# Performance work log

Hardware: AMD Instinct MI355X
Metric: run time of the kernel (lower is better)

The kernel has to match this reference:

```python
import jax, jax.numpy as jnp
import numpy as np

# Module config (matches init_kwargs shape_data=[8,32,32], pow=1, spde_type='adv_diff')
N_T, N_Y, N_X = 8, 32, 32
N = N_Y * N_X            # nb_nodes
DX = DY = DT = 1.0


def build_A(kappa, m1, m2, h11, h12, h22):
    """Dense [N,N] advection-diffusion operator A = kappa^2 I + m.grad - div(H grad),
    central differences on the n_y x n_x grid, zero-Dirichlet boundary (9-pt stencil).
    All coefficient inputs are [N] vectors (node-wise)."""
    ii, jj = jnp.divmod(jnp.arange(N), N_X)   # ii: y index, jj: x index
    rows = jnp.arange(N)
    A = jnp.zeros((N, N), dtype=kappa.dtype)
    # center
    A = A.at[rows, rows].add(kappa ** 2 + 2.0 * h11 / DX**2 + 2.0 * h22 / DY**2)

    def add(A, di, dj, coef):
        vi, vj = ii + di, jj + dj
        valid = (vi >= 0) & (vi < N_Y) & (vj >= 0) & (vj < N_X)
        cols = jnp.clip(vi, 0, N_Y - 1) * N_X + jnp.clip(vj, 0, N_X - 1)
        return A.at[rows, cols].add(jnp.where(valid, coef, 0.0))

    A = add(A, 0, +1, -h11 / DX**2 + m1 / (2.0 * DX))
    A = add(A, 0, -1, -h11 / DX**2 - m1 / (2.0 * DX))
    A = add(A, +1, 0, -h22 / DY**2 + m2 / (2.0 * DY))
    A = add(A, -1, 0, -h22 / DY**2 - m2 / (2.0 * DY))
    cxy = h12 / (2.0 * DX * DY)    # cross term -2*H12*u_xy with /(4 dx dy) stencil
    A = add(A, +1, +1, -cxy)
    A = add(A, -1, -1, -cxy)
    A = add(A, +1, -1, +cxy)
    A = add(A, -1, +1, +cxy)
    return A


def _forward(kappa, m, H, tau):
    n_b = kappa.shape[0]
    # reorder field params to [n_b, n_t, N]
    kap = jnp.moveaxis(kappa[:, 0], -1, 1)
    m1 = jnp.moveaxis(m[:, 0], -1, 1)
    m2 = jnp.moveaxis(m[:, 1], -1, 1)
    h11 = jnp.moveaxis(H[:, 0, 0], -1, 1)
    h12 = jnp.moveaxis(H[:, 0, 1], -1, 1)
    h22 = jnp.moveaxis(H[:, 1, 1], -1, 1)
    tau_ = jnp.moveaxis(tau[:, 0], -1, 1)

    flat = lambda a: a.reshape(n_b * N_T, N)
    A = jax.vmap(build_A)(flat(kap), flat(m1), flat(m2), flat(h11), flat(h12), flat(h22))
    A = A.reshape(n_b, N_T, N, N)                 # B = A since pow == 1

    eye = jnp.eye(N, dtype=A.dtype)
    M = eye + DT * A                               # inv_M_k = I + dt*B_k, [n_b,n_t,N,N]
    w = DT / (tau_ ** 2)                           # Qs_tilde_k = diag(dt / tau_k^2)

    WM = w[..., :, None] * M                       # diag(w_k) @ M_k
    P = jnp.einsum('btij,btik->btjk', M, WM)       # M_k^T diag(w_k) M_k

    # diagonal blocks: D_k = P_k + diag(w_{k+1}) for k < n_t-1; D_{n_t-1} = P_{n_t-1}
    w_next = jnp.concatenate([w[:, 1:], jnp.zeros_like(w[:, :1])], axis=1)
    D = P + w_next[..., :, None] * eye

    # sub-diagonal block (k, k-1) = -M_k^T diag(w_k), k = 1..n_t-1 (0-block padded at front)
    zblk = jnp.zeros((n_b, 1, N, N), dtype=A.dtype)
    lower = jnp.concatenate([zblk, -jnp.swapaxes(WM[:, 1:], -1, -2)], axis=1)
    # super-diagonal block (k, k+1) = -diag(w_{k+1}) M_{k+1}, k = 0..n_t-2 (0-block at end)
    upper = jnp.concatenate([-WM[:, 1:], zblk], axis=1)

    # block-tridiagonal precision Q, packed as [n_b, 3(diag,lower,upper), n_t, N, N]
    return jnp.stack([D, lower, upper], axis=1)


def setup_inputs() -> dict:
    key = jax.random.key(0)
    ks = jax.random.split(key, 4)
    n_b = 2
    kappa = 0.1 + 0.9 * jax.random.uniform(ks[0], (n_b, 1, N, N_T), dtype=jnp.float32)
    m = 0.2 * jax.random.normal(ks[1], (n_b, 2, N, N_T), dtype=jnp.float32)
    H = jax.random.uniform(ks[2], (n_b, 2, 2, N, N_T), dtype=jnp.float32)
    H = H.at[:, 0, 1].multiply(0.2)
    H = H.at[:, 1, 0].set(H[:, 0, 1])              # symmetric diffusion tensor
    tau = 0.5 + jax.random.uniform(ks[3], (n_b, 1, N, N_T), dtype=jnp.float32)
    return {"kappa": kappa, "m": m, "H": H, "tau": tau}


def reference(kappa, m, H, tau):
    return _forward(kappa, m, H, tau)
```

## Files before the change

kernel.cpp:

```cpp
#include <hip/hip_runtime.h>

#define NT 8
#define NY 32
#define NX 32
#define NN 1024

typedef __attribute__((ext_vector_type(4))) float f32x4;

__device__ __forceinline__ void node_coefs(const float* __restrict__ kap,
                                           const float* __restrict__ m,
                                           const float* __restrict__ H,
                                           const float* __restrict__ tau,
                                           int b, int node, int tc,
                                           int iy, int ix,
                                           float* c , float& w) {
    const int base = node * NT + tc;
    const float kp  = kap[(b * NN) * NT + base];
    const float m1  = m[((b * 2 + 0) * NN) * NT + base];
    const float m2  = m[((b * 2 + 1) * NN) * NT + base];
    const float h11 = H[((b * 4 + 0) * NN) * NT + base];
    const float h12 = H[((b * 4 + 1) * NN) * NT + base];
    const float h22 = H[((b * 4 + 3) * NN) * NT + base];
    const float tv  = tau[(b * NN) * NT + base];
    w = 1.0f / (tv * tv);

    const float cxy = 0.5f * h12;
    const bool ym = iy > 0, yp = iy < NY - 1;
    const bool xm = ix > 0, xp = ix < NX - 1;

    c[4] = 1.0f + kp * kp + 2.0f * h11 + 2.0f * h22;
    c[0] = (ym && xm) ? -cxy               : 0.0f;
    c[1] =  ym        ? (-h22 - 0.5f * m2) : 0.0f;
    c[2] = (ym && xp) ?  cxy               : 0.0f;
    c[3] =  xm        ? (-h11 - 0.5f * m1) : 0.0f;
    c[5] =  xp        ? (-h11 + 0.5f * m1) : 0.0f;
    c[6] = (yp && xm) ?  cxy               : 0.0f;
    c[7] =  yp        ? (-h22 + 0.5f * m2) : 0.0f;
    c[8] = (yp && xp) ? -cxy               : 0.0f;
}

__global__ __launch_bounds__(256) void spde_scatter_row(const float* __restrict__ kap,
                                                        const float* __restrict__ m,
                                                        const float* __restrict__ H,
                                                        const float* __restrict__ tau,
                                                        float* __restrict__ out) {
    __shared__ float sc[3][34][9];
    __shared__ float sw[3][34];
    __shared__ float valsD[32][25];
    __shared__ float valsL[32][9];
    __shared__ float valsU[32][9];

    const int gb  = blockIdx.x;
    const int jy  = gb & 31;
    const int t   = (gb >> 5) & 7;
    const int b   = gb >> 8;
    const int tid = threadIdx.x;

    if (tid < 102) {
        const int ly = tid / 34, lx = tid % 34;
        const int iy = jy + ly - 1, ix = lx - 1;
        float c[9];
        float w = 0.0f;
        if (iy >= 0 && iy < NY && ix >= 0 && ix < NX) {
            node_coefs(kap, m, H, tau, b, iy * NX + ix, t, iy, ix, c, w);
        } else {
            #pragma unroll
            for (int q = 0; q < 9; ++q) c[q] = 0.0f;
        }
        #pragma unroll
        for (int q = 0; q < 9; ++q) sc[ly][lx][q] = c[q];
        sw[ly][lx] = w;
    }
    __syncthreads();

    #pragma unroll
    for (int pass = 0; pass < 6; ++pass) {
        const int e = tid + pass * 256;
        if (e < 800) {
            const int jj = e / 25, l = e % 25;
            const int dy = l / 5 - 2, dx = l % 5 - 2;
            float acc = 0.0f;
            #pragma unroll
            for (int d = 0; d < 9; ++d) {
                const int ey = d / 3 - 1, ex = d % 3 - 1;
                const int r2y = dy - ey, r2x = dx - ex;
                if (r2y >= -1 && r2y <= 1 && r2x >= -1 && r2x <= 1) {
                    const float* ci = sc[ey + 1][jj + 1 + ex];
                    acc += sw[ey + 1][jj + 1 + ex] * ci[8 - d]
                }
            }
            if (l == 12 && t < NT - 1) {
                const int j = jy * NX + jj;
                const float tv = tau[((size_t)b * NN + j) * NT + (t + 1)];
                acc += 1.0f / (tv * tv);
            }
            valsD[jj][l] = acc;
        } else if (e < 1088) {
            const int e2 = e - 800;
            const int jj = e2 / 9, d = e2 % 9;
            const int ey = d / 3 - 1, ex = d % 3 - 1;
            valsL[jj][d] = -sw[ey + 1][jj + 1 + ex] * sc[ey + 1][jj + 1 + ex][8 - d];
        } else if (e < 1376) {
            const int e2 = e - 1088;
            const int jj = e2 / 9, qi = e2 % 9;
            valsU[jj][qi] = -sw[1][jj + 1] * sc[1][jj + 1][qi];
        }
    }
    __syncthreads();

    f32x4* const outq = (f32x4*)out;
    const size_t matD = ((size_t)(b * 3 + 0) * NT + t) << 18;
    const int rowbase = jy * NX;

    #pragma unroll
    for (int pass = 0; pass < 5; ++pass) {
        const int idx = tid + pass * 256;
        const int jj = idx / 40, r = idx % 40;
        const int s = r >> 3, q = r & 7;
        const int ky = jy - 2 + s;
        if (ky >= 0 && ky < NY) {
            f32x4 v = {0.f, 0.f, 0.f, 0.f};
            #pragma unroll
            for (int cq = 0; cq < 4; ++cq) {
                const int ddx = q * 4 + cq - jj;
                if (ddx >= -2 && ddx <= 2) v[cq] = valsD[jj][s * 5 + (ddx + 2)];
            }
            outq[matD + ((size_t)(rowbase + jj) << 8) + ky * 8 + q] = v;
        }
    }

    if (t >= 1) {
        const size_t matL = ((size_t)(b * 3 + 1) * NT + t) << 18;
        const size_t matU = ((size_t)(b * 3 + 2) * NT + (t - 1)) << 18;
        #pragma unroll
        for (int pass = 0; pass < 3; ++pass) {
            const int idx = tid + pass * 256;
            const int jj = idx / 24, r = idx % 24;
            const int s = r >> 3, q = r & 7;
            const int ky = jy - 1 + s;
            if (ky >= 0 && ky < NY) {
                f32x4 v = {0.f, 0.f, 0.f, 0.f};
                #pragma unroll
                for (int cq = 0; cq < 4; ++cq) {
                    const int ddx = q * 4 + cq - jj;
                    if (ddx >= -1 && ddx <= 1) v[cq] = valsL[jj][s * 3 + (ddx + 1)];
                }
                outq[matL + ((size_t)(rowbase + jj) << 8) + ky * 8 + q] = v;
            }
        }
        #pragma unroll
        for (int pass = 0; pass < 3; ++pass) {
            const int idx = tid + pass * 256;
            const int jj = idx / 24, r = idx % 24;
            const int s = r >> 3, q = r & 7;
            const int ky = jy - 1 + s;
            if (ky >= 0 && ky < NY) {
                f32x4 v = {0.f, 0.f, 0.f, 0.f};
                #pragma unroll
                for (int cq = 0; cq < 4; ++cq) {
                    const int ddx = q * 4 + cq - jj;
                    if (ddx >= -1 && ddx <= 1) v[cq] = valsU[jj][s * 3 + (ddx + 1)];
                }
                outq[matU + ((size_t)(rowbase + jj) << 8) + ky * 8 + q] = v;
            }
        }
    }
}

extern "C" void kernel_launch(void* const* d_in, const int* in_sizes, int n_in,
                              void* d_out, int out_size, void* d_ws, size_t ws_size,
                              hipStream_t stream) {
    (void)n_in; (void)d_ws; (void)ws_size;
    const float* kap = (const float*)d_in[0];
    const float* m   = (const float*)d_in[1];
    const float* H   = (const float*)d_in[2];
    const float* tau = (const float*)d_in[3];
    float* out = (float*)d_out;

    const int n_b = in_sizes[0] / (NN * NT);

    hipMemsetAsync(d_out, 0, (size_t)out_size, stream);

    const int grid = n_b * NT * NY;
    spde_scatter_row<<<grid, 256, 0, stream>>>(kap, m, H, tau, out);
}
```

Measured before the change: 191.0 us.

## Split D, L, U block writes into separate workgroups per row

Triples the grid so each workgroup handles one role: the diagonal block, the lower block, or the upper block for a given batch, time step and grid row. Upper-block workgroups compute only the 32 node coefficients they need for step t+1, and lower-block workgroups read coefficients straight from shared memory instead of staging them in separate arrays. The aim is more parallelism and shorter per-workgroup critical paths, at the cost of recomputing the shared halo coefficients in both the D and L workgroups. Runtime is likely dominated by the full-output memset, so the gain may be limited.

```diff
diff --git a/kernel.cpp b/kernel.cpp
--- a/kernel.cpp
+++ b/kernel.cpp
@@ -39,22 +39,57 @@
     c[8] = (yp && xp) ? -cxy               : 0.0f;
 }
 
-__global__ __launch_bounds__(256) void spde_scatter_row(const float* __restrict__ kap,
-                                                        const float* __restrict__ m,
-                                                        const float* __restrict__ H,
-                                                        const float* __restrict__ tau,
-                                                        float* __restrict__ out) {
+__global__ __launch_bounds__(256) void spde_scatter3(const float* __restrict__ kap,
+                                                     const float* __restrict__ m,
+                                                     const float* __restrict__ H,
+                                                     const float* __restrict__ tau,
+                                                     float* __restrict__ out) {
     __shared__ float sc[3][34][9];
     __shared__ float sw[3][34];
     __shared__ float valsD[32][25];
-    __shared__ float valsL[32][9];
-    __shared__ float valsU[32][9];
 
-    const int gb  = blockIdx.x;
-    const int jy  = gb & 31;
-    const int t   = (gb >> 5) & 7;
-    const int b   = gb >> 8;
-    const int tid = threadIdx.x;
+    const int gb   = blockIdx.x;
+    const int role = gb % 3;
+    const int rest = gb / 3;
+    const int jy   = rest & 31;
+    const int t    = (rest >> 5) & 7;
+    const int b    = rest >> 8;
+    const int tid  = threadIdx.x;
+
+    if (role == 1 && t == 0) return;
+    if (role == 2 && t == NT - 1) return;
+
+    f32x4* const outq = (f32x4*)out;
+    const int rowbase = jy * NX;
+
+    if (role == 2) {
+        if (tid < 32) {
+            float c[9];
+            float w;
+            node_coefs(kap, m, H, tau, b, jy * NX + tid, t + 1, jy, tid, c, w);
+            #pragma unroll
+            for (int q = 0; q < 9; ++q) valsD[tid][q] = -w * c[q];
+        }
+        __syncthreads();
+        const size_t matU = ((size_t)(b * 3 + 2) * NT + t) << 18;
+        #pragma unroll
+        for (int pass = 0; pass < 3; ++pass) {
+            const int idx = tid + pass * 256;
+            const int jj = idx / 24, r = idx % 24;
+            const int s = r >> 3, q = r & 7;
+            const int ky = jy - 1 + s;
+            if (ky >= 0 && ky < NY) {
+                f32x4 v = {0.f, 0.f, 0.f, 0.f};
+                #pragma unroll
+                for (int cq = 0; cq < 4; ++cq) {
+                    const int ddx = q * 4 + cq - jj;
+                    if (ddx >= -1 && ddx <= 1) v[cq] = valsD[jj][s * 3 + (ddx + 1)];
+                }
+                outq[matU + ((size_t)(rowbase + jj) << 8) + ky * 8 + q] = v;
+            }
+        }
+        return;
+    }
 
     if (tid < 102) {
         const int ly = tid / 34, lx = tid % 34;
@@ -73,65 +108,51 @@
     }
     __syncthreads();
 
-    #pragma unroll
-    for (int pass = 0; pass < 6; ++pass) {
-        const int e = tid + pass * 256;
-        if (e < 800) {
-            const int jj = e / 25, l = e % 25;
-            const int dy = l / 5 - 2, dx = l % 5 - 2;
-            float acc = 0.0f;
-            #pragma unroll
-            for (int d = 0; d < 9; ++d) {
-                const int ey = d / 3 - 1, ex = d % 3 - 1;
-                const int r2y = dy - ey, r2x = dx - ex;
-                if (r2y >= -1 && r2y <= 1 && r2x >= -1 && r2x <= 1) {
-                    const float* ci = sc[ey + 1][jj + 1 + ex];
-                    acc += sw[ey + 1][jj + 1 + ex] * ci[8 - d]
+    if (role == 0) {
+        #pragma unroll
+        for (int pass = 0; pass < 4; ++pass) {
+            const int e = tid + pass * 256;
+            if (e < 800) {
+                const int jj = e / 25, l = e % 25;
+                const int dy = l / 5 - 2, dx = l % 5 - 2;
+                float acc = 0.0f;
+                #pragma unroll
+                for (int d = 0; d < 9; ++d) {
+                    const int ey = d / 3 - 1, ex = d % 3 - 1;
+                    const int r2y = dy - ey, r2x = dx - ex;
+                    if (r2y >= -1 && r2y <= 1 && r2x >= -1 && r2x <= 1) {
+                        const float* ci = sc[ey + 1][jj + 1 + ex];
+                        acc += sw[ey + 1][jj + 1 + ex] * ci[8 - d]
+                    }
                 }
+                if (l == 12 && t < NT - 1) {
+                    const int j = rowbase + jj;
+                    const float tv = tau[((size_t)b * NN + j) * NT + (t + 1)];
+                    acc += 1.0f / (tv * tv);
+                }
+                valsD[jj][l] = acc;
             }
-            if (l == 12 && t < NT - 1) {
-                const int j = jy * NX + jj;
-                const float tv = tau[((size_t)b * NN + j) * NT + (t + 1)];
-                acc += 1.0f / (tv * tv);
+        }
+        __syncthreads();
+        const size_t matD = ((size_t)(b * 3 + 0) * NT + t) << 18;
+        #pragma unroll
+        for (int pass = 0; pass < 5; ++pass) {
+            const int idx = tid + pass * 256;
+            const int jj = idx / 40, r = idx % 40;
+            const int s = r >> 3, q = r & 7;
+            const int ky = jy - 2 + s;
+            if (ky >= 0 && ky < NY) {
+                f32x4 v = {0.f, 0.f, 0.f, 0.f};
+                #pragma unroll
+                for (int cq = 0; cq < 4; ++cq) {
+                    const int ddx = q * 4 + cq - jj;
+                    if (ddx >= -2 && ddx <= 2) v[cq] = valsD[jj][s * 5 + (ddx + 2)];
+                }
+                outq[matD + ((size_t)(rowbase + jj) << 8) + ky * 8 + q] = v;
             }
-            valsD[jj][l] = acc;
-        } else if (e < 1088) {
-            const int e2 = e - 800;
-            const int jj = e2 / 9, d = e2 % 9;
-            const int ey = d / 3 - 1, ex = d % 3 - 1;
-            valsL[jj][d] = -sw[ey + 1][jj + 1 + ex] * sc[ey + 1][jj + 1 + ex][8 - d];
-        } else if (e < 1376) {
-            const int e2 = e - 1088;
-            const int jj = e2 / 9, qi = e2 % 9;
-            valsU[jj][qi] = -sw[1][jj + 1] * sc[1][jj + 1][qi];
         }
-    }
-    __syncthreads();
-
-    f32x4* const outq = (f32x4*)out;
-    const size_t matD = ((size_t)(b * 3 + 0) * NT + t) << 18;
-    const int rowbase = jy * NX;
-
-    #pragma unroll
-    for (int pass = 0; pass < 5; ++pass) {
-        const int idx = tid + pass * 256;
-        const int jj = idx / 40, r = idx % 40;
-        const int s = r >> 3, q = r & 7;
-        const int ky = jy - 2 + s;
-        if (ky >= 0 && ky < NY) {
-            f32x4 v = {0.f, 0.f, 0.f, 0.f};
-            #pragma unroll
-            for (int cq = 0; cq < 4; ++cq) {
-                const int ddx = q * 4 + cq - jj;
-                if (ddx >= -2 && ddx <= 2) v[cq] = valsD[jj][s * 5 + (ddx + 2)];
-            }
-            outq[matD + ((size_t)(rowbase + jj) << 8) + ky * 8 + q] = v;
-        }
-    }
-
-    if (t >= 1) {
+    } else {
         const size_t matL = ((size_t)(b * 3 + 1) * NT + t) << 18;
-        const size_t matU = ((size_t)(b * 3 + 2) * NT + (t - 1)) << 18;
         #pragma unroll
         for (int pass = 0; pass < 3; ++pass) {
             const int idx = tid + pass * 256;
@@ -143,25 +164,12 @@
                 #pragma unroll
                 for (int cq = 0; cq < 4; ++cq) {
                     const int ddx = q * 4 + cq - jj;
-                    if (ddx >= -1 && ddx <= 1) v[cq] = valsL[jj][s * 3 + (ddx + 1)];
+                    if (ddx >= -1 && ddx <= 1) {
+                        const int d = s * 3 + (ddx + 1);
+                        v[cq] = -sw[s][jj + 1 + ddx] * sc[s][jj + 1 + ddx][8 - d];
+                    }
                 }
                 outq[matL + ((size_t)(rowbase + jj) << 8) + ky * 8 + q] = v;
-            }
-        }
-        #pragma unroll
-        for (int pass = 0; pass < 3; ++pass) {
-            const int idx = tid + pass * 256;
-            const int jj = idx / 24, r = idx % 24;
-            const int s = r >> 3, q = r & 7;
-            const int ky = jy - 1 + s;
-            if (ky >= 0 && ky < NY) {
-                f32x4 v = {0.f, 0.f, 0.f, 0.f};
-                #pragma unroll
-                for (int cq = 0; cq < 4; ++cq) {
-                    const int ddx = q * 4 + cq - jj;
-                    if (ddx >= -1 && ddx <= 1) v[cq] = valsU[jj][s * 3 + (ddx + 1)];
-                }
-                outq[matU + ((size_t)(rowbase + jj) << 8) + ky * 8 + q] = v;
             }
         }
     }
@@ -181,6 +189,6 @@
 
     hipMemsetAsync(d_out, 0, (size_t)out_size, stream);
 
-    const int grid = n_b * NT * NY;
-    spde_scatter_row<<<grid, 256, 0, stream>>>(kap, m, H, tau, out);
+    const int grid = n_b * NT * NY * 3;
+    spde_scatter3<<<grid, 256, 0, stream>>>(kap, m, H, tau, out);
 }
```

New measurement: 189.5 us. About the same (-0.8%).
